# Performance work log

Hardware: AMD Instinct MI355X
Metric: run time of the kernel (lower is better)

Reference implementation:

```python
import jax, jax.numpy as jnp
import numpy as np

B, L, E, H, D = 4, 2048, 2048, 16, 128
HALF = D // 2
EPS = 1e-6


def setup_inputs() -> dict:
    key = jax.random.key(0)
    ks = jax.random.split(key, 8)
    s = 1.0 / np.sqrt(E)
    x = jax.random.normal(ks[0], (B, L, E), dtype=jnp.float32)
    # causal boolean mask, True = attend
    attention_mask = jnp.tril(jnp.ones((L, L), dtype=bool))[None, None, :, :]
    attention_mask = jnp.broadcast_to(attention_mask, (B, 1, L, L))
    pos = jnp.arange(L, dtype=jnp.float32)[:, None]
    inv_freq = 1.0 / (10000.0 ** (jnp.arange(HALF, dtype=jnp.float32) / HALF))
    ang = pos * inv_freq[None, :]  # [L, HALF]
    cos = jnp.broadcast_to(jnp.cos(ang)[None], (B, L, HALF)).astype(jnp.float32)
    sin = jnp.broadcast_to(jnp.sin(ang)[None], (B, L, HALF)).astype(jnp.float32)
    Wq = jax.random.normal(ks[1], (H * D, E), dtype=jnp.float32) * s
    Wk = jax.random.normal(ks[2], (H * D, E), dtype=jnp.float32) * s
    Wv = jax.random.normal(ks[3], (H * D, E), dtype=jnp.float32) * s
    Wo = jax.random.normal(ks[4], (E, H * D), dtype=jnp.float32) * s
    q_norm_w = jnp.ones((D,), dtype=jnp.float32)
    k_norm_w = jnp.ones((D,), dtype=jnp.float32)
    return {"x": x, "attention_mask": attention_mask, "cos": cos, "sin": sin,
            "Wq": Wq, "Wk": Wk, "Wv": Wv, "Wo": Wo,
            "q_norm_w": q_norm_w, "k_norm_w": k_norm_w}


def _rmsnorm(t, w):
    # t: [B,H,L,D]; matches torch: x / sqrt(mean(x^2) + eps) * w
    ms = jnp.mean(t * t, axis=-1, keepdims=True)
    return w * (t * jax.lax.rsqrt(ms + EPS))


def _rope(t, cos, sin):
    # t: [B,H,L,D]; cos/sin: [B,L,HALF] -> [B,1,L,HALF]
    c = cos[:, None, :, :]
    s = sin[:, None, :, :]
    t1, t2 = t[..., :HALF], t[..., HALF:]
    return jnp.concatenate([t1 * c - t2 * s, t1 * s + t2 * c], axis=-1)


def reference(x, attention_mask, cos, sin, Wq, Wk, Wv, Wo, q_norm_w, k_norm_w):
    b, l, _ = x.shape
    q = (x @ Wq.T).reshape(b, l, H, D).transpose(0, 2, 1, 3)  # [B,H,L,D]
    k = (x @ Wk.T).reshape(b, l, H, D).transpose(0, 2, 1, 3)
    v = (x @ Wv.T).reshape(b, l, H, D).transpose(0, 2, 1, 3)
    q = _rope(_rmsnorm(q, q_norm_w), cos, sin)
    k = _rope(_rmsnorm(k, k_norm_w), cos, sin)
    scale = 1.0 / jnp.sqrt(jnp.asarray(D, dtype=x.dtype))
    scores = jnp.einsum('bhld,bhmd->bhlm', q, k) * scale  # [B,H,L,L]
    scores = jnp.where(attention_mask, scores, -jnp.inf)
    attn = jax.nn.softmax(scores, axis=-1)
    out = jnp.einsum('bhlm,bhmd->bhld', attn, v)  # [B,H,L,D]
    out = out.transpose(0, 2, 1, 3).reshape(b, l, H * D)
    return out @ Wo.T
```

## Files before the change

### kernel.cpp

```cpp
#include <hip/hip_runtime.h>
#include <hip/hip_bf16.h>
#include <stdint.h>

#define B_SZ 4
#define L_SEQ 2048
#define EMB 2048
#define NH 16
#define HD 128
#define BLROWS (B_SZ * L_SEQ)

typedef __bf16 bf16;
typedef __bf16 bf16x8 __attribute__((ext_vector_type(8)));
typedef __bf16 bf16x4 __attribute__((ext_vector_type(4)));
typedef float f32x4 __attribute__((ext_vector_type(4)));

#define MFMA16(A, Bv, C) __builtin_amdgcn_mfma_f32_16x16x32_bf16(A, Bv, C, 0, 0, 0)

__device__ __forceinline__ void gll16(bf16* l, const bf16* g) {
  __builtin_amdgcn_global_load_lds(
      (const __attribute__((address_space(1))) unsigned int*)g,
      (__attribute__((address_space(3))) unsigned int*)l, 16, 0, 0);
}

__global__ __launch_bounds__(256) void f2b_kernel(const float* __restrict__ in,
                                                  bf16* __restrict__ out, int n4) {
  int i = blockIdx.x * blockDim.x + threadIdx.x;
  int stride = gridDim.x * blockDim.x;
  for (; i < n4; i += stride) {
    float4 v = ((const float4*)in)[i];
    bf16x4 o = {(bf16)v.x, (bf16)v.y, (bf16)v.z, (bf16)v.w};
    ((bf16x4*)out)[i] = o;
  }
}

template <int EPI>
__global__ __launch_bounds__(512, 2) void gemm256(const bf16* __restrict__ A,
                                                  const bf16* __restrict__ Bm,
                                                  bf16* __restrict__ Cq,
                                                  bf16* __restrict__ Ck,
                                                  bf16* __restrict__ Cvt,
                                                  float* __restrict__ Cf,
                                                  int K) {
  __shared__ bf16 Abuf[2][256 * 64];
  __shared__ bf16 Bbuf[2][256 * 64];
  const int tid = threadIdx.x, lane = tid & 63, w = tid >> 6;
  const int wr = w >> 2, wc = w & 3;
  const int l15 = lane & 15;

  const int q8 = gridDim.x >> 3;
  const int wg = ((int)blockIdx.x & 7) * q8 + ((int)blockIdx.x >> 3);
  const int bm = (wg & 31) * 256;
  const int bn = (wg >> 5) * 256;
  const int NT = K >> 6;

  size_t sAg[4], sBg[4];
  int sdst[4];
#pragma unroll
  for (int g = 0; g < 4; g++) {
    int id = g * 512 + tid;
    int row = id >> 3, c = id & 7;
    int scol = ((c ^ (row & 7)) * 8);
    sAg[g] = (size_t)(bm + row) * K + scol;
    sBg[g] = (size_t)(bn + row) * K + scol;
    sdst[g] = id * 8;
  }

  int aoff[8][2], boff[4][2];
#pragma unroll
  for (int m = 0; m < 8; m++)
#pragma unroll
    for (int ks = 0; ks < 2; ks++) {
      int row = wr * 128 + m * 16 + l15;
      int cl = ks * 4 + (lane >> 4);
      aoff[m][ks] = row * 64 + ((cl ^ (row & 7)) * 8);
    }
#pragma unroll
  for (int n = 0; n < 4; n++)
#pragma unroll
    for (int ks = 0; ks < 2; ks++) {
      int row = wc * 64 + n * 16 + l15;
      int cl = ks * 4 + (lane >> 4);
      boff[n][ks] = row * 64 + ((cl ^ (row & 7)) * 8);
    }

  f32x4 acc[8][4] = {};

#pragma unroll
  for (int g = 0; g < 4; g++) {
    gll16(&Abuf[0][sdst[g]], A + sAg[g]);
    gll16(&Bbuf[0][sdst[g]], Bm + sBg[g]);
  }
  asm volatile("s_waitcnt vmcnt(0)" ::: "memory");
  __builtin_amdgcn_s_barrier();
  asm volatile("" ::: "memory");

  for (int t = 0; t < NT; ++t) {
    const bf16* __restrict__ Ab = Abuf[t & 1];
    const bf16* __restrict__ Bb = Bbuf[t & 1];
    bf16* __restrict__ An = Abuf[(t + 1) & 1];
    bf16* __restrict__ Bn = Bbuf[(t + 1) & 1];
    const size_t k1 = (size_t)(t + 1) << 6;
    const bool pre = (t + 1 < NT);

    bf16x8 bq[4][2];

#pragma unroll
    for (int mp = 0; mp < 4; mp++) {
      bf16x8 a0k0 = *(const bf16x8*)&Ab[aoff[2 * mp][0]];
      bf16x8 a0k1 = *(const bf16x8*)&Ab[aoff[2 * mp][1]];
      bf16x8 a1k0 = *(const bf16x8*)&Ab[aoff[2 * mp + 1][0]];
      bf16x8 a1k1 = *(const bf16x8*)&Ab[aoff[2 * mp + 1][1]];
      if (mp == 0) {
#pragma unroll
        for (int n = 0; n < 4; n++) {
          bq[n][0] = *(const bf16x8*)&Bb[boff[n][0]];
          bq[n][1] = *(const bf16x8*)&Bb[boff[n][1]];
        }
        if (pre) {
#pragma unroll
          for (int g = 0; g < 4; g++) {
            gll16(&An[sdst[g]], A + sAg[g] + k1);
            gll16(&Bn[sdst[g]], Bm + sBg[g] + k1);
          }
        }
      }
      __builtin_amdgcn_s_barrier();
      asm volatile("s_waitcnt lgkmcnt(0)" ::: "memory");
      __builtin_amdgcn_sched_barrier(0);
      __builtin_amdgcn_s_setprio(1);
#pragma unroll
      for (int n = 0; n < 4; n++) {
        acc[2 * mp][n] = MFMA16(a0k0, bq[n][0], acc[2 * mp][n]);
        acc[2 * mp][n] = MFMA16(a0k1, bq[n][1], acc[2 * mp][n]);
        acc[2 * mp + 1][n] = MFMA16(a1k0, bq[n][0], acc[2 * mp + 1][n]);
        acc[2 * mp + 1][n] = MFMA16(a1k1, bq[n][1], acc[2 * mp + 1][n]);
      }
      __builtin_amdgcn_s_setprio(0);
      if (mp == 3) asm volatile("s_waitcnt vmcnt(0)" ::: "memory");
      __builtin_amdgcn_s_barrier();
      asm volatile("" ::: "memory");
    }
  }

  const int grow0 = bm + wr * 128 + (lane >> 4) * 4;
  const int gcol0 = bn + wc * 64 + l15;
#pragma unroll
  for (int i = 0; i < 8; i++)
#pragma unroll
    for (int j = 0; j < 4; j++) {
      int grow = grow0 + i * 16;
      int gcol = gcol0 + j * 16;
      if (EPI == 1) {
#pragma unroll
        for (int r = 0; r < 4; r++)
          Cf[(size_t)(grow + r) * 2048 + gcol] = acc[i][j][r];
      } else {
        int mat = gcol >> 11, mcol = gcol & 2047;
        if (mat == 2) {
          int b = grow >> 11;
          bf16x4 pk = {(bf16)acc[i][j][0], (bf16)acc[i][j][1],
                       (bf16)acc[i][j][2], (bf16)acc[i][j][3]};
          *(bf16x4*)&Cvt[((size_t)(b * 2048 + mcol)) * 2048 + (grow & 2047)] = pk;
        } else {
          bf16* Cp = (mat == 0) ? Cq : Ck;
#pragma unroll
          for (int r = 0; r < 4; r++)
            Cp[(size_t)(grow + r) * 2048 + mcol] = (bf16)acc[i][j][r];
        }
      }
    }
}

__global__ __launch_bounds__(256) void normrope_kernel(bf16* __restrict__ T,
                                                       const float* __restrict__ w,
                                                       const float* __restrict__ cs,
                                                       const float* __restrict__ sn) {
  int row = blockIdx.x * 4 + (threadIdx.x >> 6);
  int lane = threadIdx.x & 63;
  int bl = row >> 4;
  int h = row & 15;
  bf16* p = T + (size_t)bl * EMB + h * HD;
  float v1 = (float)p[lane];
  float v2 = (float)p[lane + 64];
  float ss = v1 * v1 + v2 * v2;
#pragma unroll
  for (int m = 32; m; m >>= 1) ss += __shfl_xor(ss, m, 64);
  float r = rsqrtf(ss * (1.0f / 128.0f) + 1e-6f);
  float n1 = v1 * r * w[lane];
  float n2 = v2 * r * w[lane + 64];
  float c = cs[(size_t)bl * 64 + lane];
  float s = sn[(size_t)bl * 64 + lane];
  p[lane]      = (bf16)(n1 * c - n2 * s);
  p[lane + 64] = (bf16)(n1 * s + n2 * c);
}

__device__ __forceinline__ void stage_kv(bf16* Ksb, bf16* Vsb,
                                         const bf16* gK, const bf16* gV,
                                         int kt, int w, int lane) {
#pragma unroll
  for (int i = 0; i < 4; i++) {
    int ck = i * 256 + w * 64 + lane;
    int kr = ck >> 4, kc = ck & 15;
    gll16(&Ksb[ck * 8], gK + (size_t)(kt * 64 + kr) * EMB + ((kc ^ (kr & 7)) * 8));
    int dr = ck >> 3, vc = ck & 7;
    gll16(&Vsb[ck * 8], gV + (size_t)dr * L_SEQ + kt * 64 + ((vc ^ (dr & 7)) * 8));
  }
}

__global__ __launch_bounds__(256) void fattn_kernel(const bf16* __restrict__ Q,
                                                    const bf16* __restrict__ K,
                                                    const bf16* __restrict__ Vt,
                                                    bf16* __restrict__ AO) {
  __shared__ bf16 Ks[2][64 * 128];
  __shared__ bf16 Vs[2][64 * 128];
  __shared__ bf16 Ps[4 * 16 * 64];
  const int tid = threadIdx.x, lane = tid & 63, w = tid >> 6;

  int id = blockIdx.x + blockIdx.y * 32;
  int bh = id & 63;
  int qt = 31 - (id >> 6);
  const int b = bh >> 4, h = bh & 15;
  const size_t base = (size_t)b * L_SEQ * EMB + h * HD;
  const bf16* gK = K + base;
  const bf16* gV = Vt + (size_t)(b * NH + h) * HD * L_SEQ;
  const int qrow0 = qt * 64 + w * 16;

  const float a_ = 0.08838834764831845f * 1.4426950408889634f;
  const float b_ = 12.0f * 1.4426950408889634f;

  bf16x8 qf[4];
  {
    const bf16* qp = Q + base + (size_t)(qrow0 + (lane & 15)) * EMB + ((lane >> 4) * 8);
#pragma unroll
    for (int c = 0; c < 4; c++) qf[c] = *(const bf16x8*)(qp + c * 32);
  }
  const bf16 one1 = (bf16)1.0f;
  const bf16x8 ones = {one1, one1, one1, one1, one1, one1, one1, one1};

  f32x4 O[8] = {};
  f32x4 lsum = {0.f, 0.f, 0.f, 0.f};
  const int qg0 = qrow0 + (lane >> 4) * 4;
  bf16* myP = Ps + w * 1024;

  stage_kv(Ks[0], Vs[0], gK, gV, 0, w, lane);
  asm volatile("s_waitcnt vmcnt(0)" ::: "memory");
  __builtin_amdgcn_s_barrier();
  asm volatile("" ::: "memory");

  for (int kt = 0; kt <= qt; kt++) {
    const int cur = kt & 1;
    if (kt < qt) stage_kv(Ks[cur ^ 1], Vs[cur ^ 1], gK, gV, kt + 1, w, lane);

    f32x4 S[4] = {};
    __builtin_amdgcn_s_setprio(1);
#pragma unroll
    for (int s = 0; s < 4; s++) {
      int row = s * 16 + (lane & 15);
#pragma unroll
      for (int c = 0; c < 4; c++) {
        int swc = (c * 4 + (lane >> 4)) ^ (row & 7);
        bf16x8 kf = *(const bf16x8*)&Ks[cur][row * 128 + swc * 8];
        S[s] = MFMA16(qf[c], kf, S[s]);
      }
    }
    __builtin_amdgcn_s_setprio(0);

    const bool diag = (kt == qt);
    const int prow = (lane >> 4) * 4;
#pragma unroll
    for (int s = 0; s < 4; s++) {
      int kg = kt * 64 + s * 16 + (lane & 15);
#pragma unroll
      for (int r = 0; r < 4; r++) {
        float e = exp2f(S[s][r] * a_ - b_);
        if (diag && kg > qg0 + r) e = 0.f;
        int row = prow + r;
        myP[(row * 64 + s * 16 + (lane & 15)) ^ ((row & 7) << 3)] = (bf16)e;
      }
    }
    bf16x8 pf[2];
#pragma unroll
    for (int kk = 0; kk < 2; kk++) {
      int row = lane & 15;
      int swc = (kk * 4 + (lane >> 4)) ^ (row & 7);
      pf[kk] = *(const bf16x8*)&myP[row * 64 + swc * 8];
    }
    __builtin_amdgcn_s_setprio(1);
    lsum = MFMA16(pf[0], ones, lsum);
    lsum = MFMA16(pf[1], ones, lsum);
#pragma unroll
    for (int ni = 0; ni < 8; ni++) {
#pragma unroll
      for (int kk = 0; kk < 2; kk++) {
        int drow = ni * 16 + (lane & 15);
        int swc = (kk * 4 + (lane >> 4)) ^ (drow & 7);
        bf16x8 vf = *(const bf16x8*)&Vs[cur][drow * 64 + swc * 8];
        O[ni] = MFMA16(pf[kk], vf, O[ni]);
      }
    }
    __builtin_amdgcn_s_setprio(0);

    asm volatile("s_waitcnt vmcnt(0)" ::: "memory");
    __builtin_amdgcn_s_barrier();
    asm volatile("" ::: "memory");
  }

#pragma unroll
  for (int ni = 0; ni < 8; ni++) {
#pragma unroll
    for (int r = 0; r < 4; r++) {
      float o = O[ni][r] / lsum[r];
      AO[(size_t)(b * L_SEQ + qg0 + r) * EMB + h * HD + ni * 16 + (lane & 15)] = (bf16)o;
    }
  }
}

extern "C" void kernel_launch(void* const* d_in, const int* in_sizes, int n_in,
                              void* d_out, int out_size, void* d_ws, size_t ws_size,
                              hipStream_t stream) {
  const float* x = (const float*)d_in[0];
  const float* cosp = (const float*)d_in[2];
  const float* sinp = (const float*)d_in[3];
  const float* Wq = (const float*)d_in[4];
  const float* Wk = (const float*)d_in[5];
  const float* Wv = (const float*)d_in[6];
  const float* Wo = (const float*)d_in[7];
  const float* qw = (const float*)d_in[8];
  const float* kw = (const float*)d_in[9];

  const size_t ACT = (size_t)BLROWS * EMB * sizeof(bf16);
  const size_t WGT = (size_t)EMB * EMB * sizeof(bf16);
  char* ws = (char*)d_ws;
  bf16* xb    = (bf16*)ws;          ws += ACT;
  bf16* WQKVb = (bf16*)ws;          ws += 3 * WGT;
  bf16* Wob   = (bf16*)ws;          ws += WGT;
  bf16* Qb    = (bf16*)ws;          ws += ACT;
  bf16* Kb    = (bf16*)ws;          ws += ACT;
  bf16* Vtb   = (bf16*)ws;          ws += ACT;
  bf16* AOb   = (bf16*)ws;          ws += ACT;

  f2b_kernel<<<2048, 256, 0, stream>>>(x, xb, BLROWS * EMB / 4);
  f2b_kernel<<<1024, 256, 0, stream>>>(Wq, WQKVb, EMB * EMB / 4);
  f2b_kernel<<<1024, 256, 0, stream>>>(Wk, WQKVb + (size_t)EMB * EMB, EMB * EMB / 4);
  f2b_kernel<<<1024, 256, 0, stream>>>(Wv, WQKVb + 2 * (size_t)EMB * EMB, EMB * EMB / 4);
  f2b_kernel<<<1024, 256, 0, stream>>>(Wo, Wob, EMB * EMB / 4);

  gemm256<0><<<768, 512, 0, stream>>>(xb, WQKVb, Qb, Kb, Vtb, nullptr, EMB);

  normrope_kernel<<<BLROWS * NH / 4, 256, 0, stream>>>(Qb, qw, cosp, sinp);
  normrope_kernel<<<BLROWS * NH / 4, 256, 0, stream>>>(Kb, kw, cosp, sinp);

  fattn_kernel<<<dim3(32, B_SZ * NH), 256, 0, stream>>>(Qb, Kb, Vtb, AOb);

  gemm256<1><<<256, 512, 0, stream>>>(AOb, Wob, nullptr, nullptr, nullptr,
                                      (float*)d_out, EMB);
}
```

Before: 491.7 us.

## Split GEMM tile into quadrants with staggered per-half global-to-LDS prefetch

Restructures the 256x256 bf16 GEMM so each operand tile is split into two 128-row halves held in separate double-buffered LDS arrays. The k-loop now runs four quadrant MFMA phases, and each phase issues the prefetch for one half-tile, two steps ahead where possible. Partial vmcnt waits replace the single full drain per k-step. The aim is to spread global-load issue across the MFMA work and hide memory latency better. In exchange it adds more barriers per iteration and delicate vmcnt accounting that could stall or race if the counts are off.

New measurement: 492.6 us. Within noise of the previous version (+0.2%).

```diff
diff --git a/kernel.cpp b/kernel.cpp
--- a/kernel.cpp
+++ b/kernel.cpp
@@ -41,8 +41,10 @@
                                                   bf16* __restrict__ Cvt,
                                                   float* __restrict__ Cf,
                                                   int K) {
-  __shared__ bf16 Abuf[2][256 * 64];
-  __shared__ bf16 Bbuf[2][256 * 64];
+  __shared__ bf16 A0b[2][128 * 64];
+  __shared__ bf16 A1b[2][128 * 64];
+  __shared__ bf16 B0b[2][128 * 64];
+  __shared__ bf16 B1b[2][128 * 64];
   const int tid = threadIdx.x, lane = tid & 63, w = tid >> 6;
   const int wr = w >> 2, wc = w & 3;
   const int l15 = lane & 15;
@@ -53,122 +55,192 @@
   const int bn = (wg >> 5) * 256;
   const int NT = K >> 6;
 
-  size_t sAg[4], sBg[4];
-  int sdst[4];
-#pragma unroll
-  for (int g = 0; g < 4; g++) {
-    int id = g * 512 + tid;
-    int row = id >> 3, c = id & 7;
-    int scol = ((c ^ (row & 7)) * 8);
-    sAg[g] = (size_t)(bm + row) * K + scol;
-    sBg[g] = (size_t)(bn + row) * K + scol;
-    sdst[g] = id * 8;
-  }
-
-  int aoff[8][2], boff[4][2];
-#pragma unroll
-  for (int m = 0; m < 8; m++)
+  const int r0 = tid >> 3;
+  const int scol = (((tid & 7) ^ (r0 & 7)) * 8);
+  const size_t offA0 = (size_t)(bm + r0) * K + scol;
+  const size_t offA1 = offA0 + (size_t)128 * K;
+  const size_t offB0 = (size_t)(bn + r0) * K + scol;
+  const size_t offB1 = offB0 + (size_t)128 * K;
+  const size_t rstep = (size_t)64 * K;
+  const int d0 = tid * 8, d1 = 4096 + tid * 8;
+
+#define STAGE(dst, src, base, tk)                  \
+  do {                                             \
+    gll16((dst) + d0, (src) + (base) + (tk));      \
+    gll16((dst) + d1, (src) + (base) + rstep + (tk)); \
+  } while (0)
+
+  int aoff[4][2], boff[2][2];
+#pragma unroll
+  for (int m = 0; m < 4; m++)
 #pragma unroll
     for (int ks = 0; ks < 2; ks++) {
-      int row = wr * 128 + m * 16 + l15;
+      int row = wr * 64 + m * 16 + l15;
       int cl = ks * 4 + (lane >> 4);
       aoff[m][ks] = row * 64 + ((cl ^ (row & 7)) * 8);
     }
 #pragma unroll
-  for (int n = 0; n < 4; n++)
+  for (int n = 0; n < 2; n++)
 #pragma unroll
     for (int ks = 0; ks < 2; ks++) {
-      int row = wc * 64 + n * 16 + l15;
+      int row = wc * 32 + n * 16 + l15;
       int cl = ks * 4 + (lane >> 4);
       boff[n][ks] = row * 64 + ((cl ^ (row & 7)) * 8);
     }
 
-  f32x4 acc[8][4] = {};
-
-#pragma unroll
-  for (int g = 0; g < 4; g++) {
-    gll16(&Abuf[0][sdst[g]], A + sAg[g]);
-    gll16(&Bbuf[0][sdst[g]], Bm + sBg[g]);
-  }
-  asm volatile("s_waitcnt vmcnt(0)" ::: "memory");
+  f32x4 acc[2][2][4][2] = {};
+
+  STAGE(A0b[0], A, offA0, 0);
+  STAGE(B0b[0], Bm, offB0, 0);
+  STAGE(A1b[0], A, offA1, 0);
+  STAGE(B1b[0], Bm, offB1, 0);
+  STAGE(A0b[1], A, offA0, 64);
+  STAGE(B0b[1], Bm, offB0, 64);
+  STAGE(A1b[1], A, offA1, 64);
+  STAGE(B1b[1], Bm, offB1, 64);
+  asm volatile("s_waitcnt vmcnt(12)" ::: "memory");
   __builtin_amdgcn_s_barrier();
   asm volatile("" ::: "memory");
 
-  for (int t = 0; t < NT; ++t) {
-    const bf16* __restrict__ Ab = Abuf[t & 1];
-    const bf16* __restrict__ Bb = Bbuf[t & 1];
-    bf16* __restrict__ An = Abuf[(t + 1) & 1];
-    bf16* __restrict__ Bn = Bbuf[(t + 1) & 1];
-    const size_t k1 = (size_t)(t + 1) << 6;
-    const bool pre = (t + 1 < NT);
-
-    bf16x8 bq[4][2];
-
-#pragma unroll
-    for (int mp = 0; mp < 4; mp++) {
-      bf16x8 a0k0 = *(const bf16x8*)&Ab[aoff[2 * mp][0]];
-      bf16x8 a0k1 = *(const bf16x8*)&Ab[aoff[2 * mp][1]];
-      bf16x8 a1k0 = *(const bf16x8*)&Ab[aoff[2 * mp + 1][0]];
-      bf16x8 a1k1 = *(const bf16x8*)&Ab[aoff[2 * mp + 1][1]];
-      if (mp == 0) {
-#pragma unroll
-        for (int n = 0; n < 4; n++) {
-          bq[n][0] = *(const bf16x8*)&Bb[boff[n][0]];
-          bq[n][1] = *(const bf16x8*)&Bb[boff[n][1]];
-        }
-        if (pre) {
-#pragma unroll
-          for (int g = 0; g < 4; g++) {
-            gll16(&An[sdst[g]], A + sAg[g] + k1);
-            gll16(&Bn[sdst[g]], Bm + sBg[g] + k1);
+  for (int g = 0; g < NT; ++g) {
+    const int par = g & 1, parn = par ^ 1;
+    const bf16* __restrict__ Ab0 = A0b[par];
+    const bf16* __restrict__ Ab1 = A1b[par];
+    const bf16* __restrict__ Bb0 = B0b[par];
+    const bf16* __restrict__ Bb1 = B1b[par];
+    const size_t k1 = (size_t)(g + 1) << 6, k2 = (size_t)(g + 2) << 6;
+    const bool s1 = (g >= 1) && (g + 1 < NT);
+    const bool s2 = (g + 2 < NT);
+
+    bf16x8 af[4][2], bq0[2][2], bq1[2][2];
+
+#pragma unroll
+    for (int m = 0; m < 4; m++) {
+      af[m][0] = *(const bf16x8*)&Ab0[aoff[m][0]];
+      af[m][1] = *(const bf16x8*)&Ab0[aoff[m][1]];
+    }
+#pragma unroll
+    for (int n = 0; n < 2; n++) {
+      bq0[n][0] = *(const bf16x8*)&Bb0[boff[n][0]];
+      bq0[n][1] = *(const bf16x8*)&Bb0[boff[n][1]];
+    }
+    if (s1) STAGE(A1b[parn], A, offA1, k1);
+    __builtin_amdgcn_s_barrier();
+    asm volatile("s_waitcnt lgkmcnt(0)" ::: "memory");
+    __builtin_amdgcn_sched_barrier(0);
+    __builtin_amdgcn_s_setprio(1);
+#pragma unroll
+    for (int m = 0; m < 4; m++)
+#pragma unroll
+      for (int n = 0; n < 2; n++) {
+        acc[0][0][m][n] = MFMA16(af[m][0], bq0[n][0], acc[0][0][m][n]);
+        acc[0][0][m][n] = MFMA16(af[m][1], bq0[n][1], acc[0][0][m][n]);
+      }
+    __builtin_amdgcn_s_setprio(0);
+    if (g == 0)
+      asm volatile("s_waitcnt vmcnt(8)" ::: "memory");
+    else if (g + 1 < NT)
+      asm volatile("s_waitcnt vmcnt(6)" ::: "memory");
+    else
+      asm volatile("s_waitcnt vmcnt(0)" ::: "memory");
+    __builtin_amdgcn_s_barrier();
+    asm volatile("" ::: "memory");
+
+#pragma unroll
+    for (int n = 0; n < 2; n++) {
+      bq1[n][0] = *(const bf16x8*)&Bb1[boff[n][0]];
+      bq1[n][1] = *(const bf16x8*)&Bb1[boff[n][1]];
+    }
+    if (s1) STAGE(B1b[parn], Bm, offB1, k1);
+    __builtin_amdgcn_s_barrier();
+    asm volatile("s_waitcnt lgkmcnt(0)" ::: "memory");
+    __builtin_amdgcn_sched_barrier(0);
+    __builtin_amdgcn_s_setprio(1);
+#pragma unroll
+    for (int m = 0; m < 4; m++)
+#pragma unroll
+      for (int n = 0; n < 2; n++) {
+        acc[0][1][m][n] = MFMA16(af[m][0], bq1[n][0], acc[0][1][m][n]);
+        acc[0][1][m][n] = MFMA16(af[m][1], bq1[n][1], acc[0][1][m][n]);
+      }
+    __builtin_amdgcn_s_setprio(0);
+    __builtin_amdgcn_s_barrier();
+    asm volatile("" ::: "memory");
+
+#pragma unroll
+    for (int m = 0; m < 4; m++) {
+      af[m][0] = *(const bf16x8*)&Ab1[aoff[m][0]];
+      af[m][1] = *(const bf16x8*)&Ab1[aoff[m][1]];
+    }
+    if (s2) STAGE(A0b[par], A, offA0, k2);
+    __builtin_amdgcn_s_barrier();
+    asm volatile("s_waitcnt lgkmcnt(0)" ::: "memory");
+    __builtin_amdgcn_sched_barrier(0);
+    __builtin_amdgcn_s_setprio(1);
+#pragma unroll
+    for (int m = 0; m < 4; m++)
+#pragma unroll
+      for (int n = 0; n < 2; n++) {
+        acc[1][0][m][n] = MFMA16(af[m][0], bq0[n][0], acc[1][0][m][n]);
+        acc[1][0][m][n] = MFMA16(af[m][1], bq0[n][1], acc[1][0][m][n]);
+      }
+    __builtin_amdgcn_s_setprio(0);
+    __builtin_amdgcn_s_barrier();
+    asm volatile("" ::: "memory");
+
+    if (s2) STAGE(B0b[par], Bm, offB0, k2);
+    __builtin_amdgcn_s_barrier();
+    asm volatile("s_waitcnt lgkmcnt(0)" ::: "memory");
+    __builtin_amdgcn_sched_barrier(0);
+    __builtin_amdgcn_s_setprio(1);
+#pragma unroll
+    for (int m = 0; m < 4; m++)
+#pragma unroll
+      for (int n = 0; n < 2; n++) {
+        acc[1][1][m][n] = MFMA16(af[m][0], bq1[n][0], acc[1][1][m][n]);
+        acc[1][1][m][n] = MFMA16(af[m][1], bq1[n][1], acc[1][1][m][n]);
+      }
+    __builtin_amdgcn_s_setprio(0);
+    if (g + 1 < NT) {
+      if (g + 2 < NT)
+        asm volatile("s_waitcnt vmcnt(8)" ::: "memory");
+      else
+        asm volatile("s_waitcnt vmcnt(4)" ::: "memory");
+    }
+    __builtin_amdgcn_s_barrier();
+    asm volatile("" ::: "memory");
+  }
+#undef STAGE
+
+#pragma unroll
+  for (int qm = 0; qm < 2; qm++)
+#pragma unroll
+    for (int qn = 0; qn < 2; qn++)
+#pragma unroll
+      for (int m = 0; m < 4; m++)
+#pragma unroll
+        for (int n = 0; n < 2; n++) {
+          int grow = bm + qm * 128 + wr * 64 + m * 16 + (lane >> 4) * 4;
+          int gcol = bn + qn * 128 + wc * 32 + n * 16 + l15;
+          f32x4 v = acc[qm][qn][m][n];
+          if (EPI == 1) {
+#pragma unroll
+            for (int r = 0; r < 4; r++)
+              Cf[(size_t)(grow + r) * 2048 + gcol] = v[r];
+          } else {
+            int mat = gcol >> 11, mcol = gcol & 2047;
+            if (mat == 2) {
+              int b = grow >> 11;
+              bf16x4 pk = {(bf16)v[0], (bf16)v[1], (bf16)v[2], (bf16)v[3]};
+              *(bf16x4*)&Cvt[((size_t)(b * 2048 + mcol)) * 2048 + (grow & 2047)] = pk;
+            } else {
+              bf16* Cp = (mat == 0) ? Cq : Ck;
+#pragma unroll
+              for (int r = 0; r < 4; r++)
+                Cp[(size_t)(grow + r) * 2048 + mcol] = (bf16)v[r];
+            }
           }
         }
-      }
-      __builtin_amdgcn_s_barrier();
-      asm volatile("s_waitcnt lgkmcnt(0)" ::: "memory");
-      __builtin_amdgcn_sched_barrier(0);
-      __builtin_amdgcn_s_setprio(1);
-#pragma unroll
-      for (int n = 0; n < 4; n++) {
-        acc[2 * mp][n] = MFMA16(a0k0, bq[n][0], acc[2 * mp][n]);
-        acc[2 * mp][n] = MFMA16(a0k1, bq[n][1], acc[2 * mp][n]);
-        acc[2 * mp + 1][n] = MFMA16(a1k0, bq[n][0], acc[2 * mp + 1][n]);
-        acc[2 * mp + 1][n] = MFMA16(a1k1, bq[n][1], acc[2 * mp + 1][n]);
-      }
-      __builtin_amdgcn_s_setprio(0);
-      if (mp == 3) asm volatile("s_waitcnt vmcnt(0)" ::: "memory");
-      __builtin_amdgcn_s_barrier();
-      asm volatile("" ::: "memory");
-    }
-  }
-
-  const int grow0 = bm + wr * 128 + (lane >> 4) * 4;
-  const int gcol0 = bn + wc * 64 + l15;
-#pragma unroll
-  for (int i = 0; i < 8; i++)
-#pragma unroll
-    for (int j = 0; j < 4; j++) {
-      int grow = grow0 + i * 16;
-      int gcol = gcol0 + j * 16;
-      if (EPI == 1) {
-#pragma unroll
-        for (int r = 0; r < 4; r++)
-          Cf[(size_t)(grow + r) * 2048 + gcol] = acc[i][j][r];
-      } else {
-        int mat = gcol >> 11, mcol = gcol & 2047;
-        if (mat == 2) {
-          int b = grow >> 11;
-          bf16x4 pk = {(bf16)acc[i][j][0], (bf16)acc[i][j][1],
-                       (bf16)acc[i][j][2], (bf16)acc[i][j][3]};
-          *(bf16x4*)&Cvt[((size_t)(b * 2048 + mcol)) * 2048 + (grow & 2047)] = pk;
-        } else {
-          bf16* Cp = (mat == 0) ? Cq : Ck;
-#pragma unroll
-          for (int r = 0; r < 4; r++)
-            Cp[(size_t)(grow + r) * 2048 + mcol] = (bf16)acc[i][j][r];
-        }
-      }
-    }
 }
 
 __global__ __launch_bounds__(256) void normrope_kernel(bf16* __restrict__ T,
```
